# Kernel tuning notes

Measured on AMD Instinct MI355X. Metric: run time of the kernel, lower is better.

Reference implementation:

```python
import jax, jax.numpy as jnp
import numpy as np

B, S, K, H = 512, 128, 4, 128  # batch, seq_len, interest_num, hidden_size
ROUTING_TIMES = 3
EPS = 1e-9


def setup_inputs() -> dict:
    key = jax.random.key(0)
    k1, k2 = jax.random.split(key)
    item_eb = jax.random.normal(k1, (B, S, H), dtype=jnp.float32)
    mask = jnp.ones((B, S), dtype=jnp.float32)
    # learned bilinear map parameter (bilinear_type == 2)
    w = jax.random.normal(k2, (1, S, K * H, H), dtype=jnp.float32) * 0.02
    return {"item_eb": item_eb, "mask": mask, "w": w}


def _squash(cap):
    # cap: [B, K, 1, H]
    n = jnp.sum(cap * cap, axis=-1, keepdims=True)
    return (n / (1.0 + n) / jnp.sqrt(n + EPS)) * cap


def reference(item_eb, mask, w):
    # bilinear_type==2: sum(w[:, :S] * item_eb[:, :, None, :], axis=3)
    # expressed as an einsum to avoid the [B,S,K*H,H] intermediate
    item_eb_hat = jnp.einsum('bsh,sdh->bsd', item_eb, w[0])          # [B, S, K*H]
    item_eb_hat = item_eb_hat.reshape(B, S, K, H).transpose(0, 2, 1, 3)  # [B, K, S, H]
    hat_iter = jax.lax.stop_gradient(item_eb_hat)  # stop_grad=True

    atten_mask = jnp.broadcast_to(mask[:, None, :], (B, K, S))
    capsule_weight = jnp.zeros((B, K, S), dtype=item_eb.dtype)  # bilinear_type > 0

    interest_capsule = None
    for i in range(ROUTING_TIMES):
        # torch F.softmax with implicit dim on a 3D tensor -> dim=0 (legacy)
        sw = jax.nn.softmax(capsule_weight, axis=0)
        sw = jnp.where(atten_mask == 0, 0.0, sw)[:, :, None, :]  # [B, K, 1, S]
        src = hat_iter if i < 2 else item_eb_hat
        interest_capsule = _squash(jnp.matmul(sw, src))  # [B, K, 1, H]
        if i < 2:
            delta = jnp.matmul(hat_iter, interest_capsule.transpose(0, 1, 3, 2))  # [B,K,S,1]
            capsule_weight = capsule_weight + delta.reshape(B, K, S)

    return interest_capsule.reshape(B, K, H)
```

## Files before the change

### kernel.cpp

```cpp
#include <hip/hip_runtime.h>
#include <math.h>

#define BB 512
#define SS 128
#define KK 4
#define HH 128
#define DD 512

typedef __attribute__((ext_vector_type(8))) short bf16x8;
typedef __attribute__((ext_vector_type(4))) float f32x4;

__device__ __forceinline__ unsigned short f2bf(float f) {
  unsigned u = __float_as_uint(f);
  unsigned r = u + 0x7fffu + ((u >> 16) & 1u);
  return (unsigned short)(r >> 16);
}
__device__ __forceinline__ ushort4 f2bf4(float4 v) {
  ushort4 o; o.x = f2bf(v.x); o.y = f2bf(v.y); o.z = f2bf(v.z); o.w = f2bf(v.w);
  return o;
}
__device__ __forceinline__ float bfhi(unsigned u) { return __uint_as_float(u & 0xffff0000u); }
__device__ __forceinline__ float bflo(unsigned u) { return __uint_as_float(u << 16); }

__device__ __forceinline__ void async_cp16(const void* g, void* l) {
  __builtin_amdgcn_global_load_lds(
      (const __attribute__((address_space(1))) unsigned int*)g,
      (__attribute__((address_space(3))) unsigned int*)l, 16, 0, 0);
}

__global__ __launch_bounds__(256) void einsum_mfma(
    const float* __restrict__ item,
    const float* __restrict__ w,
    unsigned short* __restrict__ hat)
{
  __shared__ unsigned short Al[128 * 128];
  __shared__ unsigned short Wl[2][128 * 64];
  const int s  = blockIdx.x;
  const int b0 = blockIdx.y * 128;
  const int t  = threadIdx.x;
  const int lane = t & 63, wvq = t >> 6;
  const int qm = wvq & 1, qn = wvq >> 1;
  const int n16 = lane & 15, kq = lane >> 4;

  const float* Abase = item + ((size_t)b0 * SS + s) * HH;
  const float* Wbase = w + (size_t)s * DD * HH;

  const int ac = t & 31, ar0 = t >> 5;
  const int wc = t & 15, wr0 = t >> 4;
  float4 apre[16];
  #pragma unroll
  for (int j = 0; j < 16; ++j)
    apre[j] = *(const float4*)(Abase + (size_t)(ar0 + 8 * j) * (SS * HH) + ac * 4);
  float4 wpre[8];
  #pragma unroll
  for (int j = 0; j < 8; ++j)
    wpre[j] = *(const float4*)(Wbase + (size_t)(wr0 + 16 * j) * HH + wc * 4);

  #pragma unroll
  for (int j = 0; j < 16; ++j) {
    const int r = ar0 + 8 * j;
    const int lg = ac >> 1;
    *(ushort4*)&Al[r * 128 + ((lg ^ (r & 15)) * 8) + (ac & 1) * 4] = f2bf4(apre[j]);
  }
  #pragma unroll
  for (int j = 0; j < 8; ++j) {
    const int r = wr0 + 16 * j;
    *(ushort4*)&Wl[0][r * 64 + ((((wc >> 1) + r) & 7) * 8) + (wc & 1) * 4] = f2bf4(wpre[j]);
  }
  __syncthreads();

  const int sx = s & 15;
  int buf = 0;
  for (int dt = 0; dt < 4; ++dt) {
    f32x4 acc[4][4] = {};
    #pragma unroll
    for (int hs = 0; hs < 2; ++hs) {
      const int step = dt * 2 + hs;
      if (step < 7) {
        const int d0n = ((step + 1) >> 1) * 128;
        const int ksn = ((step + 1) & 1) * 64;
        #pragma unroll
        for (int j = 0; j < 8; ++j)
          wpre[j] = *(const float4*)(Wbase + (size_t)(d0n + wr0 + 16 * j) * HH + ksn + wc * 4);
      }
      #pragma unroll
      for (int kk = 0; kk < 2; ++kk) {
        bf16x8 af[4], bfr[4];
        #pragma unroll
        for (int i = 0; i < 4; ++i) {
          const int ra = qm * 64 + i * 16 + n16;
          const int rb = qn * 64 + i * 16 + n16;
          af[i]  = *(const bf16x8*)&Wl[buf][ra * 64 + ((kk * 4 + kq + ra) & 7) * 8];
          bfr[i] = *(const bf16x8*)&Al[rb * 128 + (((hs * 8 + kk * 4 + kq) ^ (rb & 15)) * 8)];
        }
        #pragma unroll
        for (int i = 0; i < 4; ++i)
          #pragma unroll
          for (int j = 0; j < 4; ++j)
            acc[i][j] = __builtin_amdgcn_mfma_f32_16x16x32_bf16(af[i], bfr[j], acc[i][j], 0, 0, 0);
      }
      if (step < 7) {
        #pragma unroll
        for (int j = 0; j < 8; ++j) {
          const int r = wr0 + 16 * j;
          *(ushort4*)&Wl[buf ^ 1][r * 64 + ((((wc >> 1) + r) & 7) * 8) + (wc & 1) * 4] = f2bf4(wpre[j]);
        }
        __syncthreads();
        buf ^= 1;
      }
    }
    #pragma unroll
    for (int j = 0; j < 4; ++j) {
      const int b = b0 + qn * 64 + j * 16 + n16;
      char* orow = (char*)(hat + (((size_t)b * KK + dt) * SS + s) * HH);
      #pragma unroll
      for (int i = 0; i < 4; ++i) {
        const int h = qm * 64 + i * 16 + kq * 4;
        ushort4 o;
        o.x = f2bf(acc[i][j][0]); o.y = f2bf(acc[i][j][1]);
        o.z = f2bf(acc[i][j][2]); o.w = f2bf(acc[i][j][3]);
        *(ushort4*)(orow + ((((h >> 3) ^ sx) << 4) | ((h & 4) << 1))) = o;
      }
    }
  }
}

__global__ __launch_bounds__(256) void softmax_k(
    const float* __restrict__ cw, const float* __restrict__ mask,
    float* __restrict__ sw)
{
  __shared__ float rbuf[4];
  const int s = blockIdx.x, k = blockIdx.y, t = threadIdx.x;
  const size_t base = ((size_t)k * SS + s) * BB;
  float v0 = cw[base + t], v1 = cw[base + 256 + t];
  float m = fmaxf(v0, v1);
  #pragma unroll
  for (int o = 32; o; o >>= 1) m = fmaxf(m, __shfl_xor(m, o));
  if ((t & 63) == 0) rbuf[t >> 6] = m;
  __syncthreads();
  m = fmaxf(fmaxf(rbuf[0], rbuf[1]), fmaxf(rbuf[2], rbuf[3]));
  float e0 = expf(v0 - m), e1 = expf(v1 - m);
  float ssum = e0 + e1;
  #pragma unroll
  for (int o = 32; o; o >>= 1) ssum += __shfl_xor(ssum, o);
  __syncthreads();
  if ((t & 63) == 0) rbuf[t >> 6] = ssum;
  __syncthreads();
  float inv = 1.f / (rbuf[0] + rbuf[1] + rbuf[2] + rbuf[3]);
  float m0 = mask[(size_t)t * SS + s];
  float m1 = mask[(size_t)(t + 256) * SS + s];
  sw[base + t]       = (m0 == 0.f) ? 0.f : e0 * inv;
  sw[base + 256 + t] = (m1 == 0.f) ? 0.f : e1 * inv;
}

__global__ __launch_bounds__(256) void routing_k(
    const unsigned short* __restrict__ hat, const float* __restrict__ mask,
    const float* __restrict__ sw_in, float* __restrict__ cw,
    float* __restrict__ out, int mode)
{
  __shared__ unsigned short hat_l[128 * 128];
  __shared__ float sw_l[128];
  __shared__ float4 red4[8][32];
  __shared__ float4 cq4[32];
  const int b = blockIdx.x, k = blockIdx.y, t = threadIdx.x;
  const int wv = t >> 6, lane = t & 63;

  const char* slab = (const char*)(hat + ((size_t)b * KK + k) * SS * HH) + wv * 8192;
  char* ldst = (char*)hat_l + wv * 8192;
  #pragma unroll
  for (int j = 0; j < 8; ++j)
    async_cp16(slab + j * 1024 + lane * 16, ldst + j * 1024);

  if (lane < 32) {
    const int sv = wv * 32 + lane;
    sw_l[sv] = (mode == 0)
      ? ((mask[(size_t)b * SS + sv] == 0.f) ? 0.f : (1.f / 512.f))
      : sw_in[((size_t)k * SS + sv) * BB + b];
  }
  asm volatile("s_waitcnt vmcnt(0) lgkmcnt(0)" ::: "memory");

  {
    const int h4 = t & 31, sg = t >> 5;
    const char* base = (const char*)hat_l;
    float4 a = make_float4(0.f, 0.f, 0.f, 0.f);
    #pragma unroll 4
    for (int i = 0; i < 16; i++) {
      const int sr = sg * 16 + i;
      uint2 v = *(const uint2*)(base + sr * 256 +
                 ((((h4 >> 1) ^ (sr & 15)) << 4) | ((h4 & 1) << 3)));
      float wv2 = sw_l[sr];
      a.x = fmaf(wv2, bflo(v.x), a.x);
      a.y = fmaf(wv2, bfhi(v.x), a.y);
      a.z = fmaf(wv2, bflo(v.y), a.z);
      a.w = fmaf(wv2, bfhi(v.y), a.w);
    }
    red4[sg][h4] = a;
  }
  __syncthreads();

  if (t < 32) {
    float4 cap = red4[0][t];
    #pragma unroll
    for (int sg = 1; sg < 8; sg++) {
      float4 r = red4[sg][t];
      cap.x += r.x; cap.y += r.y; cap.z += r.z; cap.w += r.w;
    }
    float sq = cap.x * cap.x + cap.y * cap.y + cap.z * cap.z + cap.w * cap.w;
    #pragma unroll
    for (int o = 16; o; o >>= 1) sq += __shfl_xor(sq, o);
    const float n = sq;
    const float fac = n / (1.f + n) / sqrtf(n + 1e-9f);
    cap.x *= fac; cap.y *= fac; cap.z *= fac; cap.w *= fac;
    cq4[t] = cap;
    if (mode == 2)
      ((float4*)(out + ((size_t)b * KK + k) * HH))[t] = cap;
  }

  if (mode < 2) {
    __syncthreads();
    const int sr = t >> 1, hh = t & 1;
    const char* rowp = (const char*)hat_l + sr * 256;
    const int sx = sr & 15;
    float d = 0.f;
    #pragma unroll
    for (int j = 0; j < 8; j++) {
      uint4 v = *(const uint4*)(rowp + (((hh * 8 + j) ^ sx) << 4));
      float4 qa = cq4[hh * 16 + 2 * j];
      float4 qb = cq4[hh * 16 + 2 * j + 1];
      d += bflo(v.x) * qa.x + bfhi(v.x) * qa.y
         + bflo(v.y) * qa.z + bfhi(v.y) * qa.w
         + bflo(v.z) * qb.x + bfhi(v.z) * qb.y
         + bflo(v.w) * qb.z + bfhi(v.w) * qb.w;
    }
    d += __shfl_xor(d, 1);
    if (hh == 0) {
      float* p = cw + ((size_t)k * SS + sr) * BB + b;
      if (mode == 0) *p = d; else *p += d;
    }
  }
}

extern "C" void kernel_launch(void* const* d_in, const int* in_sizes, int n_in,
                              void* d_out, int out_size, void* d_ws, size_t ws_size,
                              hipStream_t stream) {
  const float* item_eb = (const float*)d_in[0];
  const float* mask    = (const float*)d_in[1];
  const float* w       = (const float*)d_in[2];
  float* out = (float*)d_out;

  char* ws = (char*)d_ws;
  unsigned short* hat_bf = (unsigned short*)ws;
  float* cw  = (float*)(ws + 67108864);
  float* swb = (float*)(ws + 68157440);

  einsum_mfma<<<dim3(128, 4), 256, 0, stream>>>(item_eb, w, hat_bf);

  routing_k<<<dim3(BB, KK), 256, 0, stream>>>(hat_bf, mask, nullptr, cw, out, 0);
  softmax_k<<<dim3(SS, KK), 256, 0, stream>>>(cw, mask, swb);
  routing_k<<<dim3(BB, KK), 256, 0, stream>>>(hat_bf, mask, swb, cw, out, 1);
  softmax_k<<<dim3(SS, KK), 256, 0, stream>>>(cw, mask, swb);
  routing_k<<<dim3(BB, KK), 256, 0, stream>>>(hat_bf, mask, swb, cw, out, 2);
}
```

Measured before the change: 172.2 us.

## Load W fragments directly from global into MFMA registers, drop W LDS staging

```diff
diff --git a/kernel.cpp b/kernel.cpp
--- a/kernel.cpp
+++ b/kernel.cpp
@@ -34,7 +34,6 @@
     unsigned short* __restrict__ hat)
 {
   __shared__ unsigned short Al[128 * 128];
-  __shared__ unsigned short Wl[2][128 * 64];
   const int s  = blockIdx.x;
   const int b0 = blockIdx.y * 128;
   const int t  = threadIdx.x;
@@ -46,68 +45,45 @@
   const float* Wbase = w + (size_t)s * DD * HH;
 
   const int ac = t & 31, ar0 = t >> 5;
-  const int wc = t & 15, wr0 = t >> 4;
-  float4 apre[16];
-  #pragma unroll
-  for (int j = 0; j < 16; ++j)
-    apre[j] = *(const float4*)(Abase + (size_t)(ar0 + 8 * j) * (SS * HH) + ac * 4);
-  float4 wpre[8];
-  #pragma unroll
-  for (int j = 0; j < 8; ++j)
-    wpre[j] = *(const float4*)(Wbase + (size_t)(wr0 + 16 * j) * HH + wc * 4);
-
-  #pragma unroll
-  for (int j = 0; j < 16; ++j) {
-    const int r = ar0 + 8 * j;
-    const int lg = ac >> 1;
-    *(ushort4*)&Al[r * 128 + ((lg ^ (r & 15)) * 8) + (ac & 1) * 4] = f2bf4(apre[j]);
-  }
-  #pragma unroll
-  for (int j = 0; j < 8; ++j) {
-    const int r = wr0 + 16 * j;
-    *(ushort4*)&Wl[0][r * 64 + ((((wc >> 1) + r) & 7) * 8) + (wc & 1) * 4] = f2bf4(wpre[j]);
+  #pragma unroll
+  for (int c = 0; c < 2; ++c) {
+    float4 ap[8];
+    #pragma unroll
+    for (int j = 0; j < 8; ++j)
+      ap[j] = *(const float4*)(Abase + (size_t)(ar0 + 8 * (c * 8 + j)) * (SS * HH) + ac * 4);
+    #pragma unroll
+    for (int j = 0; j < 8; ++j) {
+      const int r = ar0 + 8 * (c * 8 + j);
+      const int lg = ac >> 1;
+      *(ushort4*)&Al[r * 128 + ((lg ^ (r & 15)) * 8) + (ac & 1) * 4] = f2bf4(ap[j]);
+    }
   }
   __syncthreads();
 
   const int sx = s & 15;
-  int buf = 0;
   for (int dt = 0; dt < 4; ++dt) {
+    const int d0 = dt * 128;
     f32x4 acc[4][4] = {};
     #pragma unroll
-    for (int hs = 0; hs < 2; ++hs) {
-      const int step = dt * 2 + hs;
-      if (step < 7) {
-        const int d0n = ((step + 1) >> 1) * 128;
-        const int ksn = ((step + 1) & 1) * 64;
-        #pragma unroll
-        for (int j = 0; j < 8; ++j)
-          wpre[j] = *(const float4*)(Wbase + (size_t)(d0n + wr0 + 16 * j) * HH + ksn + wc * 4);
+    for (int kk4 = 0; kk4 < 4; ++kk4) {
+      bf16x8 af[4], bfr[4];
+      #pragma unroll
+      for (int i = 0; i < 4; ++i) {
+        const int ra = qm * 64 + i * 16 + n16;
+        const float* wp = Wbase + (size_t)(d0 + ra) * HH + kk4 * 32 + kq * 8;
+        float4 x = *(const float4*)wp;
+        float4 y = *(const float4*)(wp + 4);
+        union { ushort4 q[2]; bf16x8 v; } u;
+        u.q[0] = f2bf4(x); u.q[1] = f2bf4(y);
+        af[i] = u.v;
+        const int rb = qn * 64 + i * 16 + n16;
+        bfr[i] = *(const bf16x8*)&Al[rb * 128 + (((kk4 * 4 + kq) ^ (rb & 15)) * 8)];
       }
       #pragma unroll
-      for (int kk = 0; kk < 2; ++kk) {
-        bf16x8 af[4], bfr[4];
+      for (int i = 0; i < 4; ++i)
         #pragma unroll
-        for (int i = 0; i < 4; ++i) {
-          const int ra = qm * 64 + i * 16 + n16;
-          const int rb = qn * 64 + i * 16 + n16;
-          af[i]  = *(const bf16x8*)&Wl[buf][ra * 64 + ((kk * 4 + kq + ra) & 7) * 8];
-          bfr[i] = *(const bf16x8*)&Al[rb * 128 + (((hs * 8 + kk * 4 + kq) ^ (rb & 15)) * 8)];
-        }
-        #pragma unroll
-        for (int i = 0; i < 4; ++i)
-          #pragma unroll
-          for (int j = 0; j < 4; ++j)
-            acc[i][j] = __builtin_amdgcn_mfma_f32_16x16x32_bf16(af[i], bfr[j], acc[i][j], 0, 0, 0);
-      }
-      if (step < 7) {
-        #pragma unroll
-        for (int j = 0; j < 8; ++j) {
-          const int r = wr0 + 16 * j;
-          *(ushort4*)&Wl[buf ^ 1][r * 64 + ((((wc >> 1) + r) & 7) * 8) + (wc & 1) * 4] = f2bf4(wpre[j]);
-        }
-        __syncthreads();
-        buf ^= 1;
-      }
+        for (int j = 0; j < 4; ++j)
+          acc[i][j] = __builtin_amdgcn_mfma_f32_16x16x32_bf16(af[i], bfr[j], acc[i][j], 0, 0, 0);
     }
     #pragma unroll
     for (int j = 0; j < 4; ++j) {
```

After: 205.3 us. 19.2% more time.
